# Kernel optimization log

Measured on AMD Instinct MI355X. Metric: run time of the kernel, lower is better.

The kernel has to match this reference:

```python
import jax, jax.numpy as jnp
from jax import lax
import numpy as np

L = 19  # box window size (odd -> symmetric reflect pad of L//2)


def setup_inputs() -> dict:
    key = jax.random.key(0)
    x = jax.random.normal(key, (16, 3, 1024, 1024), dtype=jnp.float32)
    return {"input": x}


def reference(input) -> jnp.ndarray:
    # BatchBlur_SV_test with l=19, padmode='reflection':
    # reflect-pad by l//2 on each side, then l x l sliding-window box sum
    # (unfold -> sum(-1) -> fold is exactly a box-sum with ones kernel).
    p = L // 2
    xp = jnp.pad(input, ((0, 0), (0, 0), (p, p), (p, p)), mode="reflect")
    out = lax.reduce_window(
        xp,
        jnp.asarray(0.0, dtype=input.dtype),
        lax.add,
        window_dimensions=(1, 1, L, L),
        window_strides=(1, 1, 1, 1),
        padding="VALID",
    )
    return out  # [B, C, H, W]
```

## Files before the change

kernel.cpp:

```cpp
#include <hip/hip_runtime.h>


#define H    1024
#define W    1024
#define RAD  9
#define KW   19
#define YSEG 128
#define NT   256

__device__ __forceinline__ int reflecti(int i, int n) {
    i = (i < 0) ? -i : i;
    return (i > n - 1) ? (2 * (n - 1) - i) : i;
}

template<int CTRL, int RMASK>
__device__ __forceinline__ float dpp_add(float s) {
    int t = __builtin_amdgcn_update_dpp(0, __float_as_int(s), CTRL, RMASK, 0xf, true);
    return s + __int_as_float(t);
}

__device__ __forceinline__ float wave_prefix_incl(float x) {
    x = dpp_add<0x111, 0xf>(x);
    x = dpp_add<0x112, 0xf>(x);
    x = dpp_add<0x114, 0xf>(x);
    x = dpp_add<0x118, 0xf>(x);
    x = dpp_add<0x142, 0xa>(x);
    x = dpp_add<0x143, 0xc>(x);
    return x;
}

__global__ __launch_bounds__(NT)
__attribute__((amdgpu_waves_per_eu(4, 5)))
void boxsum19_kernel(const float* __restrict__ in, float* __restrict__ out) {
    const int lane = threadIdx.x & 63;
    const int wid  = threadIdx.x >> 6;

    const int flat  = blockIdx.x;
    const int wg    = (flat & 7) * 192 + (flat >> 3);
    const int img   = wg >> 5;
    const int rem   = wg & 31;
    const int by    = rem >> 4;
    const int strip = rem & 15;

    const int x0 = strip * 64;
    const int y0 = (by * 4 + wid) * YSEG;
    const size_t img_off = (size_t)img * (size_t)(H * W);
    const float* __restrict__ inp  = in  + img_off;
    float* __restrict__       outp = out + img_off;

    const int gxa = reflecti(x0 - 16 + lane, W);
    const int gxb = reflecti(x0 + 48 + lane, W);
    const bool ld_b = (lane < 25);
    const int  i6   = ((lane + 6)  & 63) << 2;
    const int  i25  = ((lane + 25) & 63) << 2;
    const bool c6   = lane < 6;
    const bool c25  = lane < 25;
    const int  outcol = x0 + lane;

    float ea[KW], eb[KW], ring[KW];
    float vsum = 0.f;

#define LOADROW(trow, slot) do {                                         \
        const int gy_ = reflecti(y0 - RAD + (trow), H);                  \
        const float* rp_ = inp + ((size_t)gy_ << 10);                    \
        ea[slot] = rp_[gxa];                                             \
        if (ld_b) eb[slot] = rp_[gxb];                                   \
    } while (0)

#define HSTART(slot, q, r) do {                                          \
        float Pa_ = wave_prefix_incl(ea[slot]);                          \
        float Pb_ = wave_prefix_incl(eb[slot]);                          \
        const float At_ = __int_as_float(                                \
            __builtin_amdgcn_readlane(__float_as_int(Pa_), 63));         \
        Pb_ += At_;                                                      \
        const float mq_ = c6  ? Pb_ : Pa_;                               \
        const float mr_ = c25 ? Pb_ : Pa_;                               \
        q = __int_as_float(                                              \
            __builtin_amdgcn_ds_bpermute(i6,  __float_as_int(mq_)));     \
        r = __int_as_float(                                              \
            __builtin_amdgcn_ds_bpermute(i25, __float_as_int(mr_)));     \
    } while (0)

    #pragma unroll
    for (int j = 0; j < KW; ++j) eb[j] = 0.f;

    #pragma unroll
    for (int j = 0; j < KW; ++j) LOADROW(j, j);

    #pragma unroll
    for (int j = 0; j < KW - 1; ++j) {
        float q_, r_; HSTART(j, q_, r_);
        const float h = r_ - q_;
        LOADROW(j + KW, j);
        ring[j] = h;
        vsum += h;
    }

    float qc, rc;
    HSTART(18, qc, rc);

    int t = KW - 1;
    for (int blk = 0; blk < 6; ++blk) {
        #pragma unroll
        for (int j = 0; j < KW; ++j) {
            const int slot = (KW - 1 + j) % KW;
            const float h = rc - qc;
            HSTART(j, qc, rc);
            LOADROW(t + KW, slot);
            vsum += h;
            outp[(size_t)(y0 + t - (KW - 1)) * W + outcol] = vsum;
            vsum -= ring[j];
            ring[slot] = h;
            ++t;
        }
    }

    #pragma unroll
    for (int j = 0; j < YSEG - 6 * KW; ++j) {
        const int slot = (KW - 1 + j) % KW;
        const float h = rc - qc;
        if (j < YSEG - 6 * KW - 1) {
            HSTART(j, qc, rc);
        }
        vsum += h;
        outp[(size_t)(y0 + t - (KW - 1)) * W + outcol] = vsum;
        vsum -= ring[j];
        ring[slot] = h;
        ++t;
    }

#undef LOADROW
#undef HSTART
}

extern "C" void kernel_launch(void* const* d_in, const int* in_sizes, int n_in,
                              void* d_out, int out_size, void* d_ws, size_t ws_size,
                              hipStream_t stream) {
    const float* in = (const float*)d_in[0];
    float* out = (float*)d_out;
    dim3 grid(16 * 2 * 48, 1, 1);
    boxsum19_kernel<<<grid, NT, 0, stream>>>(in, out);
}
```

Before: 93.74 us.

## Use inline-asm buffer loads with scalar row offsets and explicit vmcnt waits

```diff
diff --git a/kernel.cpp b/kernel.cpp
--- a/kernel.cpp
+++ b/kernel.cpp
@@ -7,6 +7,8 @@
 #define KW   19
 #define YSEG 128
 #define NT   256
+
+typedef __attribute__((ext_vector_type(4))) unsigned int uint32x4;
 
 __device__ __forceinline__ int reflecti(int i, int n) {
     i = (i < 0) ? -i : i;
@@ -29,8 +31,7 @@
     return x;
 }
 
-__global__ __launch_bounds__(NT)
-__attribute__((amdgpu_waves_per_eu(4, 5)))
+__global__ __launch_bounds__(NT, 4)
 void boxsum19_kernel(const float* __restrict__ in, float* __restrict__ out) {
     const int lane = threadIdx.x & 63;
     const int wid  = threadIdx.x >> 6;
@@ -42,15 +43,20 @@
     const int by    = rem >> 4;
     const int strip = rem & 15;
 
-    const int x0 = strip * 64;
-    const int y0 = (by * 4 + wid) * YSEG;
+    const int x0  = strip * 64;
+    const int y0r = __builtin_amdgcn_readfirstlane((by * 4 + wid) * YSEG);
     const size_t img_off = (size_t)img * (size_t)(H * W);
     const float* __restrict__ inp  = in  + img_off;
     float* __restrict__       outp = out + img_off;
 
+    const unsigned long long ipu = (unsigned long long)(uintptr_t)inp;
+    const uint32x4 srsrc = { (unsigned)ipu, (unsigned)(ipu >> 32),
+                             (unsigned)(H * W * 4), 0x00020000u };
+
     const int gxa = reflecti(x0 - 16 + lane, W);
-    const int gxb = reflecti(x0 + 48 + lane, W);
-    const bool ld_b = (lane < 25);
+    const int gxb = reflecti(x0 + 48 + (lane < 25 ? lane : 24), W);
+    const int voffa = gxa << 2;
+    const int voffb = gxb << 2;
     const int  i6   = ((lane + 6)  & 63) << 2;
     const int  i25  = ((lane + 25) & 63) << 2;
     const bool c6   = lane < 6;
@@ -61,10 +67,18 @@
     float vsum = 0.f;
 
 #define LOADROW(trow, slot) do {                                         \
-        const int gy_ = reflecti(y0 - RAD + (trow), H);                  \
-        const float* rp_ = inp + ((size_t)gy_ << 10);                    \
-        ea[slot] = rp_[gxa];                                             \
-        if (ld_b) eb[slot] = rp_[gxb];                                   \
+        int gy_ = y0r - RAD + (trow);                                    \
+        gy_ = (gy_ < 0) ? -gy_ : ((gy_ > H - 1) ? (2 * (H - 1) - gy_) : gy_); \
+        const unsigned so_ = (unsigned)gy_ << 12;                        \
+        asm volatile("buffer_load_dword %0, %1, %2, %3 offen"            \
+            : "=v"(ea[slot]) : "v"(voffa), "s"(srsrc), "s"(so_));        \
+        asm volatile("buffer_load_dword %0, %1, %2, %3 offen"            \
+            : "=v"(eb[slot]) : "v"(voffb), "s"(srsrc), "s"(so_));        \
+    } while (0)
+
+#define WAITVM(N) do {                                                   \
+        asm volatile("s_waitcnt vmcnt(" #N ")");                         \
+        __builtin_amdgcn_sched_barrier(0);                               \
     } while (0)
 
 #define HSTART(slot, q, r) do {                                          \
@@ -82,13 +96,11 @@
     } while (0)
 
     #pragma unroll
-    for (int j = 0; j < KW; ++j) eb[j] = 0.f;
-
-    #pragma unroll
     for (int j = 0; j < KW; ++j) LOADROW(j, j);
 
     #pragma unroll
     for (int j = 0; j < KW - 1; ++j) {
+        WAITVM(34);
         float q_, r_; HSTART(j, q_, r_);
         const float h = r_ - q_;
         LOADROW(j + KW, j);
@@ -96,6 +108,7 @@
         vsum += h;
     }
 
+    WAITVM(34);
     float qc, rc;
     HSTART(18, qc, rc);
 
@@ -104,17 +117,19 @@
         #pragma unroll
         for (int j = 0; j < KW; ++j) {
             const int slot = (KW - 1 + j) % KW;
+            WAITVM(34);
             const float h = rc - qc;
             HSTART(j, qc, rc);
             LOADROW(t + KW, slot);
             vsum += h;
-            outp[(size_t)(y0 + t - (KW - 1)) * W + outcol] = vsum;
+            outp[(size_t)(y0r + t - (KW - 1)) * W + outcol] = vsum;
             vsum -= ring[j];
             ring[slot] = h;
             ++t;
         }
     }
 
+    WAITVM(0);
     #pragma unroll
     for (int j = 0; j < YSEG - 6 * KW; ++j) {
         const int slot = (KW - 1 + j) % KW;
@@ -123,13 +138,14 @@
             HSTART(j, qc, rc);
         }
         vsum += h;
-        outp[(size_t)(y0 + t - (KW - 1)) * W + outcol] = vsum;
+        outp[(size_t)(y0r + t - (KW - 1)) * W + outcol] = vsum;
         vsum -= ring[j];
         ring[slot] = h;
         ++t;
     }
 
 #undef LOADROW
+#undef WAITVM
 #undef HSTART
 }
 
```

Result: faster. 88.70 us (-5.4%).
